# Optimization experiments

Measured on AMD Instinct MI355X. Metric: run time of the kernel, lower is better.

The kernel has to match this reference:

```python
import jax, jax.numpy as jnp
import numpy as np

D = 2048
H = 16
HD = D // H


def setup_inputs() -> dict:
    key = jax.random.key(0)
    k1, k2, k3 = jax.random.split(key, 3)
    x = jax.random.normal(k1, (2, 2048, D), dtype=jnp.float32)
    # torch Linear(d, 3d, bias=False): y = x @ W.T; store transposed weight [D, 3D]
    Wqkv = jax.random.normal(k2, (D, 3 * D), dtype=jnp.float32) * (D ** -0.5)
    Wo = jax.random.normal(k3, (D, D), dtype=jnp.float32) * (D ** -0.5)
    return {"x": x, "Wqkv": Wqkv, "Wo": Wo}


def reference(x, Wqkv, Wo):
    B, S, _ = x.shape
    qkv = (x @ Wqkv).reshape(B, S, 3, H, HD)
    q = qkv[:, :, 0].transpose(0, 2, 1, 3)  # [B,H,S,HD]
    k = qkv[:, :, 1].transpose(0, 2, 1, 3)
    v = qkv[:, :, 2].transpose(0, 2, 1, 3)
    scores = jnp.einsum("bhqd,bhkd->bhqk", q, k) * (HD ** -0.5)
    causal = jnp.tril(jnp.ones((S, S), dtype=bool))  # keep lower triangle
    scores = jnp.where(causal, scores, jnp.float32(-1e9))
    a = jax.nn.softmax(scores, axis=-1)
    o = jnp.einsum("bhqk,bhkd->bhqd", a, v)
    o = o.transpose(0, 2, 1, 3).reshape(B, S, H * HD)
    return o @ Wo
```

## Files before the change

### kernel.cpp

```cpp
#include <hip/hip_runtime.h>
#include <hip/hip_bf16.h>
#include <cstdint>

typedef __bf16 bf16;
typedef __bf16 bf16x8 __attribute__((ext_vector_type(8)));
typedef __bf16 bf16x4 __attribute__((ext_vector_type(4)));
typedef float floatx4 __attribute__((ext_vector_type(4)));
typedef float f32x16 __attribute__((ext_vector_type(16)));

#define MFMA16(a, b, c) __builtin_amdgcn_mfma_f32_16x16x32_bf16(a, b, c, 0, 0, 0)
#define MFMA32(a, b, c) __builtin_amdgcn_mfma_f32_32x32x16_bf16(a, b, c, 0, 0, 0)

__device__ __forceinline__ void gload_lds16(const void* g, void* l) {
    __builtin_amdgcn_global_load_lds(
        (const __attribute__((address_space(1))) void*)g,
        (__attribute__((address_space(3))) void*)l, 16, 0, 0);
}

__global__ void downcast_kernel(const float* __restrict__ in, bf16* __restrict__ out,
                                size_t n) {
    const size_t i = ((size_t)blockIdx.x * blockDim.x + threadIdx.x) * 4;
    if (i >= n) return;
    const float4 v = *(const float4*)(in + i);
    bf16x4 o = {(bf16)v.x, (bf16)v.y, (bf16)v.z, (bf16)v.w};
    *(bf16x4*)(out + i) = o;
}

__global__ void transpose_kernel(const float* __restrict__ in, bf16* __restrict__ out,
                                 int R, int C) {
    __shared__ float tile[32][33];
    const int c0 = blockIdx.x * 32, r0 = blockIdx.y * 32;
    const int tx = threadIdx.x & 31, ty = threadIdx.x >> 5;
    for (int i = 0; i < 32; i += 8)
        tile[ty + i][tx] = in[(size_t)(r0 + ty + i) * C + (c0 + tx)];
    __syncthreads();
    for (int i = 0; i < 32; i += 8)
        out[(size_t)(c0 + ty + i) * R + (r0 + tx)] = (bf16)tile[tx][ty + i];
}

template <int MODE>
__global__ __launch_bounds__(256) void gemm_bt_kernel(
    const bf16* __restrict__ A, const bf16* __restrict__ BT,
    int M, int N, int K,
    bf16* __restrict__ qt, bf16* __restrict__ kt, bf16* __restrict__ vt,
    float* __restrict__ Cout) {
    __shared__ alignas(16) bf16 As[128 * 64];
    __shared__ alignas(16) bf16 Bs[128 * 64];

    const int tid = threadIdx.x;
    const int wave = tid >> 6, lane = tid & 63;
    const int quad = lane >> 4, r16 = lane & 15;
    const int m0 = blockIdx.y * 128, n0 = blockIdx.x * 128;
    const int wm = (wave >> 1) * 64, wn = (wave & 1) * 64;

    int srow[4], soff[4];
#pragma unroll
    for (int j = 0; j < 4; ++j) {
        const int c = tid + j * 256;
        srow[j] = c >> 3;
        soff[j] = ((c & 7) ^ (srow[j] & 7)) * 8;
    }

    floatx4 acc[4][4] = {};

    for (int k0 = 0; k0 < K; k0 += 64) {
        __syncthreads();
#pragma unroll
        for (int j = 0; j < 4; ++j) {
            const int c = tid + j * 256;
            gload_lds16(A + (size_t)(m0 + srow[j]) * K + k0 + soff[j], As + c * 8);
            gload_lds16(BT + (size_t)(n0 + srow[j]) * K + k0 + soff[j], Bs + c * 8);
        }
        __syncthreads();

#pragma unroll
        for (int kc = 0; kc < 2; ++kc) {
            bf16x8 a[4], b[4];
#pragma unroll
            for (int i = 0; i < 4; ++i) {
                const int row = wm + i * 16 + r16;
                const int sp = (4 * kc + quad) ^ (row & 7);
                a[i] = *(const bf16x8*)(As + row * 64 + sp * 8);
            }
#pragma unroll
            for (int j = 0; j < 4; ++j) {
                const int row = wn + j * 16 + r16;
                const int sp = (4 * kc + quad) ^ (row & 7);
                b[j] = *(const bf16x8*)(Bs + row * 64 + sp * 8);
            }
#pragma unroll
            for (int i = 0; i < 4; ++i)
#pragma unroll
                for (int j = 0; j < 4; ++j)
                    acc[i][j] = MFMA16(a[i], b[j], acc[i][j]);
        }
    }

    if (MODE == 0) {
        const int t = n0 >> 11;
        const float qscale = 0.08838834764831845f;
#pragma unroll
        for (int i = 0; i < 4; ++i) {
            const int mbase = m0 + wm + i * 16 + quad * 4;
            const int b_ = mbase >> 11;
            const int s = mbase & 2047;
#pragma unroll
            for (int j = 0; j < 4; ++j) {
                const int n = n0 + wn + j * 16 + r16;
                const int h = (n >> 7) & 15, hd = n & 127;
                const int bh = b_ * 16 + h;
                if (t == 0) {
#pragma unroll
                    for (int r = 0; r < 4; ++r)
                        qt[(size_t)(bh * 2048 + s + r) * 128 + hd] =
                            (bf16)(acc[i][j][r] * qscale);
                } else if (t == 1) {
#pragma unroll
                    for (int r = 0; r < 4; ++r)
                        kt[(size_t)(bh * 2048 + s + r) * 128 + hd] = (bf16)acc[i][j][r];
                } else {
                    bf16x4 pv = {(bf16)acc[i][j][0], (bf16)acc[i][j][1],
                                 (bf16)acc[i][j][2], (bf16)acc[i][j][3]};
                    *(bf16x4*)(vt + (size_t)(bh * 128 + hd) * 2048 + s) = pv;
                }
            }
        }
    } else {
#pragma unroll
        for (int i = 0; i < 4; ++i) {
            const int mbase = m0 + wm + i * 16 + quad * 4;
#pragma unroll
            for (int j = 0; j < 4; ++j) {
                const int n = n0 + wn + j * 16 + r16;
#pragma unroll
                for (int r = 0; r < 4; ++r)
                    Cout[(size_t)(mbase + r) * N + n] = acc[i][j][r];
            }
        }
    }
}

__global__ __launch_bounds__(256, 2) void attn_kernel(
    const bf16* __restrict__ qt, const bf16* __restrict__ kt,
    const bf16* __restrict__ vt, bf16* __restrict__ o) {
    __shared__ alignas(16) bf16 Ks[2][64 * 128];
    __shared__ alignas(16) bf16 Vts[2][128 * 64];
    __shared__ alignas(16) bf16 Ps[4][32 * 64];

    const int tid = threadIdx.x;
    const int wave = tid >> 6, lane = tid & 63;
    const int l31 = lane & 31, h = lane >> 5;
    const int bh = blockIdx.x, by = blockIdx.y;
    const int t = by < 8 ? by : 23 - by;
    const int b_ = bh >> 4, hh = bh & 15;

    const int q0 = t * 128;
    const int qbase = q0 + wave * 32;

    bf16x8 aq[8];
    {
        const bf16* qrow = qt + (((size_t)bh * 2048 + qbase + l31) << 7);
#pragma unroll
        for (int s = 0; s < 8; ++s)
            aq[s] = *(const bf16x8*)(qrow + s * 16 + h * 8);
    }

    auto stageKV = [&](int buf, int k0) {
#pragma unroll
        for (int j = 0; j < 4; ++j) {
            const int c = tid + j * 256;
            const int row = c >> 4, sp = c & 15, s = sp ^ (row & 15);
            gload_lds16(kt + (((size_t)bh * 2048 + k0 + row) << 7) + s * 8,
                        &Ks[buf][c * 8]);
        }
#pragma unroll
        for (int j = 0; j < 4; ++j) {
            const int c = tid + j * 256;
            const int row = c >> 3, sp = c & 7, s = sp ^ (row & 7);
            gload_lds16(vt + ((size_t)bh * 128 + row) * 2048 + k0 + s * 8,
                        &Vts[buf][c * 8]);
        }
    };

    f32x16 oacc[4] = {};
    float lsum[16] = {};

    const int nit = 2 * t + 2;
    stageKV(0, 0);
    __syncthreads();
    int cur = 0;

    for (int it = 0; it < nit; ++it) {
        if (it + 1 < nit) stageKV(cur ^ 1, (it + 1) * 64);
        const int k0 = it * 64;

        if (k0 <= qbase + 31) {
            const bf16* Kc = &Ks[cur][0];
            const bf16* Vc = &Vts[cur][0];

            f32x16 sacc[2] = {};
            __builtin_amdgcn_s_setprio(1);
#pragma unroll
            for (int nt = 0; nt < 2; ++nt) {
#pragma unroll
                for (int s = 0; s < 8; ++s) {
                    const int sp = (2 * s + h) ^ (lane & 15);
                    bf16x8 bk = *(const bf16x8*)(Kc + (nt * 32 + l31) * 128 + sp * 8);
                    sacc[nt] = MFMA32(aq[s], bk, sacc[nt]);
                }
            }
            __builtin_amdgcn_s_setprio(0);

            const bool needmask = (k0 + 63) > qbase;
#pragma unroll
            for (int nt = 0; nt < 2; ++nt) {
                const int key = k0 + nt * 32 + l31;
                const int seg0 = nt * 4 + (l31 >> 3);
#pragma unroll
                for (int r = 0; r < 16; ++r) {
                    const int rr = (r & 3) + 8 * (r >> 2) + 4 * h;
                    float e = __expf(sacc[nt][r]);
                    if (needmask && (key > qbase + rr)) e = 0.f;
                    lsum[r] += e;
                    Ps[wave][rr * 64 + ((seg0 ^ (rr & 7)) << 3) + (l31 & 7)] = (bf16)e;
                }
            }

            bf16x8 ap[4];
#pragma unroll
            for (int ks = 0; ks < 4; ++ks) {
                const int sp = (2 * ks + h) ^ (l31 & 7);
                ap[ks] = *(const bf16x8*)(&Ps[wave][l31 * 64 + sp * 8]);
            }
            __builtin_amdgcn_s_setprio(1);
#pragma unroll
            for (int d0 = 0; d0 < 4; ++d0) {
#pragma unroll
                for (int ks = 0; ks < 4; ++ks) {
                    const int sp = (2 * ks + h) ^ (l31 & 7);
                    bf16x8 bv = *(const bf16x8*)(Vc + (d0 * 32 + l31) * 64 + sp * 8);
                    oacc[d0] = MFMA32(ap[ks], bv, oacc[d0]);
                }
            }
            __builtin_amdgcn_s_setprio(0);
        }

        __syncthreads();
        cur ^= 1;
    }

#pragma unroll
    for (int r = 0; r < 16; ++r) {
        float s = lsum[r];
#pragma unroll
        for (int off = 1; off < 32; off <<= 1) s += __shfl_xor(s, off);
        lsum[r] = 1.0f / s;
    }

#pragma unroll
    for (int d0 = 0; d0 < 4; ++d0) {
#pragma unroll
        for (int r = 0; r < 16; ++r) {
            const int rr = (r & 3) + 8 * (r >> 2) + 4 * h;
            o[(size_t)(b_ * 2048 + qbase + rr) * 2048 + hh * 128 + d0 * 32 + l31] =
                (bf16)(oacc[d0][r] * lsum[r]);
        }
    }
}

extern "C" void kernel_launch(void* const* d_in, const int* in_sizes, int n_in,
                              void* d_out, int out_size, void* d_ws, size_t ws_size,
                              hipStream_t stream) {
    const float* x    = (const float*)d_in[0];
    const float* Wqkv = (const float*)d_in[1];
    const float* Wo   = (const float*)d_in[2];
    float* out        = (float*)d_out;

    char* ws = (char*)d_ws;
    bf16* xb    = (bf16*)ws; ws += (size_t)4096 * 2048 * 2;
    bf16* WqkvT = (bf16*)ws; ws += (size_t)6144 * 2048 * 2;
    bf16* WoT   = (bf16*)ws; ws += (size_t)2048 * 2048 * 2;
    bf16* qt    = (bf16*)ws; ws += (size_t)32 * 2048 * 128 * 2;
    bf16* kt    = (bf16*)ws; ws += (size_t)32 * 2048 * 128 * 2;
    bf16* vt    = (bf16*)ws; ws += (size_t)32 * 128 * 2048 * 2;
    bf16* ob    = (bf16*)ws; ws += (size_t)4096 * 2048 * 2;

    downcast_kernel<<<8192, 256, 0, stream>>>(x, xb, (size_t)4096 * 2048);
    transpose_kernel<<<dim3(192, 64), 256, 0, stream>>>(Wqkv, WqkvT, 2048, 6144);
    transpose_kernel<<<dim3(64, 64), 256, 0, stream>>>(Wo, WoT, 2048, 2048);

    gemm_bt_kernel<0><<<dim3(48, 32), 256, 0, stream>>>(
        xb, WqkvT, 4096, 6144, 2048, qt, kt, vt, nullptr);

    attn_kernel<<<dim3(32, 16), 256, 0, stream>>>(qt, kt, vt, ob);

    gemm_bt_kernel<1><<<dim3(16, 32), 256, 0, stream>>>(
        ob, WoT, 4096, 2048, 2048, nullptr, nullptr, nullptr, out);
}
```

Baseline: 375.8 us.

## Compute transposed S so P stays in registers, removing LDS round-trip

Swaps the MFMA operands so the score tile comes out transposed, with each lane holding one query row's scores across keys. The exponentiated probabilities are then packed to bf16 and exchanged between lane halves with a shuffle, forming the PV A-operand directly in registers instead of writing P to shared memory and reading it back. The row sum becomes one scalar per lane, reduced with a single shuffle and broadcast back by shuffles at the end. This frees the Ps LDS buffer and its store/load traffic, at the cost of extra cross-lane shuffles and select logic.

```diff
diff --git a/kernel.cpp b/kernel.cpp
--- a/kernel.cpp
+++ b/kernel.cpp
@@ -5,8 +5,10 @@
 typedef __bf16 bf16;
 typedef __bf16 bf16x8 __attribute__((ext_vector_type(8)));
 typedef __bf16 bf16x4 __attribute__((ext_vector_type(4)));
+typedef __bf16 bf16x2 __attribute__((ext_vector_type(2)));
 typedef float floatx4 __attribute__((ext_vector_type(4)));
 typedef float f32x16 __attribute__((ext_vector_type(16)));
+typedef int intx4 __attribute__((ext_vector_type(4)));
 
 #define MFMA16(a, b, c) __builtin_amdgcn_mfma_f32_16x16x32_bf16(a, b, c, 0, 0, 0)
 #define MFMA32(a, b, c) __builtin_amdgcn_mfma_f32_32x32x16_bf16(a, b, c, 0, 0, 0)
@@ -15,6 +17,13 @@
     __builtin_amdgcn_global_load_lds(
         (const __attribute__((address_space(1))) void*)g,
         (__attribute__((address_space(3))) void*)l, 16, 0, 0);
+}
+
+__device__ __forceinline__ int pack2(float a, float b) {
+    union { bf16x2 v; int u; } z;
+    z.v[0] = (bf16)a;
+    z.v[1] = (bf16)b;
+    return z.u;
 }
 
 __global__ void downcast_kernel(const float* __restrict__ in, bf16* __restrict__ out,
@@ -145,7 +154,6 @@
     const bf16* __restrict__ vt, bf16* __restrict__ o) {
     __shared__ alignas(16) bf16 Ks[2][64 * 128];
     __shared__ alignas(16) bf16 Vts[2][128 * 64];
-    __shared__ alignas(16) bf16 Ps[4][32 * 64];
 
     const int tid = threadIdx.x;
     const int wave = tid >> 6, lane = tid & 63;
@@ -156,13 +164,14 @@
 
     const int q0 = t * 128;
     const int qbase = q0 + wave * 32;
+    const int qrow = qbase + l31;
 
     bf16x8 aq[8];
     {
-        const bf16* qrow = qt + (((size_t)bh * 2048 + qbase + l31) << 7);
+        const bf16* qr = qt + (((size_t)bh * 2048 + qrow) << 7);
 #pragma unroll
         for (int s = 0; s < 8; ++s)
-            aq[s] = *(const bf16x8*)(qrow + s * 16 + h * 8);
+            aq[s] = *(const bf16x8*)(qr + s * 16 + h * 8);
     }
 
     auto stageKV = [&](int buf, int k0) {
@@ -183,7 +192,7 @@
     };
 
     f32x16 oacc[4] = {};
-    float lsum[16] = {};
+    float lsum = 0.f;
 
     const int nit = 2 * t + 2;
     stageKV(0, 0);
@@ -204,34 +213,41 @@
             for (int nt = 0; nt < 2; ++nt) {
 #pragma unroll
                 for (int s = 0; s < 8; ++s) {
-                    const int sp = (2 * s + h) ^ (lane & 15);
+                    const int sp = (2 * s + h) ^ (l31 & 15);
                     bf16x8 bk = *(const bf16x8*)(Kc + (nt * 32 + l31) * 128 + sp * 8);
-                    sacc[nt] = MFMA32(aq[s], bk, sacc[nt]);
+                    sacc[nt] = MFMA32(bk, aq[s], sacc[nt]);
                 }
             }
             __builtin_amdgcn_s_setprio(0);
 
             const bool needmask = (k0 + 63) > qbase;
-#pragma unroll
-            for (int nt = 0; nt < 2; ++nt) {
-                const int key = k0 + nt * 32 + l31;
-                const int seg0 = nt * 4 + (l31 >> 3);
-#pragma unroll
-                for (int r = 0; r < 16; ++r) {
-                    const int rr = (r & 3) + 8 * (r >> 2) + 4 * h;
-                    float e = __expf(sacc[nt][r]);
-                    if (needmask && (key > qbase + rr)) e = 0.f;
-                    lsum[r] += e;
-                    Ps[wave][rr * 64 + ((seg0 ^ (rr & 7)) << 3) + (l31 & 7)] = (bf16)e;
+            bf16x8 ap[4];
+#pragma unroll
+            for (int s4 = 0; s4 < 4; ++s4) {
+                const int nt = s4 >> 1, base = (s4 & 1) * 8;
+                float e[8];
+#pragma unroll
+                for (int k = 0; k < 8; ++k) {
+                    const int c = base + k;
+                    const int key = k0 + nt * 32 + (c & 3) + 8 * (c >> 2) + 4 * h;
+                    float v = __expf(sacc[nt][c]);
+                    if (needmask && key > qrow) v = 0.f;
+                    e[k] = v;
+                    lsum += v;
                 }
-            }
-
-            bf16x8 ap[4];
-#pragma unroll
-            for (int ks = 0; ks < 4; ++ks) {
-                const int sp = (2 * ks + h) ^ (l31 & 7);
-                ap[ks] = *(const bf16x8*)(&Ps[wave][l31 * 64 + sp * 8]);
-            }
+                const int X0 = pack2(e[0], e[1]), X1 = pack2(e[2], e[3]);
+                const int Y0 = pack2(e[4], e[5]), Y1 = pack2(e[6], e[7]);
+                int W0 = h ? X0 : Y0, W1 = h ? X1 : Y1;
+                W0 = __shfl_xor(W0, 32);
+                W1 = __shfl_xor(W1, 32);
+                union { intx4 w; bf16x8 v; } u;
+                u.w[0] = h ? W0 : X0;
+                u.w[1] = h ? W1 : X1;
+                u.w[2] = h ? Y0 : W0;
+                u.w[3] = h ? Y1 : W1;
+                ap[s4] = u.v;
+            }
+
             __builtin_amdgcn_s_setprio(1);
 #pragma unroll
             for (int d0 = 0; d0 < 4; ++d0) {
@@ -249,13 +265,12 @@
         cur ^= 1;
     }
 
-#pragma unroll
-    for (int r = 0; r < 16; ++r) {
-        float s = lsum[r];
-#pragma unroll
-        for (int off = 1; off < 32; off <<= 1) s += __shfl_xor(s, off);
-        lsum[r] = 1.0f / s;
-    }
+    lsum += __shfl_xor(lsum, 32);
+    const float inv = 1.0f / lsum;
+    float invr[16];
+#pragma unroll
+    for (int r = 0; r < 16; ++r)
+        invr[r] = __shfl(inv, (r & 3) + 8 * (r >> 2) + 4 * h, 32);
 
 #pragma unroll
     for (int d0 = 0; d0 < 4; ++d0) {
@@ -263,7 +278,7 @@
         for (int r = 0; r < 16; ++r) {
             const int rr = (r & 3) + 8 * (r >> 2) + 4 * h;
             o[(size_t)(b_ * 2048 + qbase + rr) * 2048 + hh * 128 + d0 * 32 + l31] =
-                (bf16)(oacc[d0][r] * lsum[r]);
+                (bf16)(oacc[d0][r] * invr[r]);
         }
     }
 }
```

Result: no change. 375.2 us (-0.2%).
